# Optimization experiments

Hardware: AMD Instinct MI355X
Metric: run time of the kernel (lower is better)

## Reference

```python
import jax, jax.numpy as jnp
import numpy as np

# Model/config dims (Llama-3-8B style attention, GQA 32q/8kv)
B, S, HID = 4, 512, 4096
NH, NKV, D = 32, 8, 128
CAP = 2048          # KV cache capacity
MAXPOS = 2048       # max_position_embeddings
START = 1024        # kvcache_start_index (uniform across batch -> static masking)
EPS = 1e-6
QK_SCALE = 1.0 / float(D) ** 0.5
NEG = -1e9


def setup_inputs() -> dict:
    key = jax.random.key(0)
    ks = jax.random.split(key, 8)
    w = 0.02  # weight init scale
    return {
        'hidden_states': jax.random.normal(ks[0], (B, S, HID), jnp.float32),
        'k_cache': jax.random.normal(ks[1], (B, NKV, CAP, D), jnp.float32),
        'v_cache': jax.random.normal(ks[2], (B, NKV, CAP, D), jnp.float32),
        'rope_rotary_cos_sin': jax.random.uniform(ks[3], (B, MAXPOS, D), jnp.float32),
        'context_lengths': jnp.full((B,), S, jnp.int32),
        'kvcache_start_index': jnp.full((B,), START, jnp.int32),
        'Wq': jax.random.normal(ks[4], (HID, NH * D), jnp.float32) * w,
        'Wk': jax.random.normal(ks[5], (HID, NKV * D), jnp.float32) * w,
        'Wv': jax.random.normal(ks[6], (HID, NKV * D), jnp.float32) * w,
        'Wo': jax.random.normal(ks[7], (NH * D, HID), jnp.float32) * w,
        'q_norm_w': jnp.ones((D,), jnp.float32),
        'k_norm_w': jnp.ones((D,), jnp.float32),
    }


def _rmsnorm(x, w):
    # per-head RMSNorm over head_dim (Qwen3-style QK norm)
    return x * jax.lax.rsqrt(jnp.mean(x * x, axis=-1, keepdims=True) + EPS) * w


def _apply_rope(x, cos, sin, pos):
    # x: [B,H,S,D]; cos/sin: [MAXPOS, D/2]; pos: [B,S]
    c = cos[pos][:, None, :, :]  # [B,1,S,D/2]
    s = sin[pos][:, None, :, :]
    x1, x2 = jnp.split(x, 2, axis=-1)
    return jnp.concatenate([x1 * c - x2 * s, x2 * c + x1 * s], axis=-1)


def reference(hidden_states, k_cache, v_cache, rope_rotary_cos_sin,
              context_lengths, kvcache_start_index,
              Wq, Wk, Wv, Wo, q_norm_w, k_norm_w):
    b, s, _ = hidden_states.shape
    # fused QKV projection
    q = (hidden_states @ Wq).reshape(b, s, NH, D)
    k = (hidden_states @ Wk).reshape(b, s, NKV, D)
    v = (hidden_states @ Wv).reshape(b, s, NKV, D)
    # QK norm
    q = _rmsnorm(q, q_norm_w)
    k = _rmsnorm(k, k_norm_w)
    # [B,H,S,D]
    q = q.transpose(0, 2, 1, 3)
    k = k.transpose(0, 2, 1, 3)
    v = v.transpose(0, 2, 1, 3)
    # RoPE tables: first half cos, second half sin; batch dim 0 only
    half = D // 2
    cos = rope_rotary_cos_sin[0, :, :half]
    sin = rope_rotary_cos_sin[0, :, half:]
    pos = kvcache_start_index[:, None] + jnp.arange(s, dtype=kvcache_start_index.dtype)[None, :]
    q = _apply_rope(q, cos, sin, pos)
    k = _apply_rope(k, cos, sin, pos)
    # KV cache update: write new k/v at per-batch start index
    def upd(cache, new, st):  # cache [H,CAP,D], new [H,S,D]
        return jax.lax.dynamic_update_slice(cache, new, (0, st, 0))
    present_k = jax.vmap(upd)(k_cache, k, kvcache_start_index)
    present_v = jax.vmap(upd)(v_cache, v, kvcache_start_index)
    # GQA: expand kv heads to attention heads
    g = NH // NKV
    kf = jnp.repeat(present_k, g, axis=1)  # [B,NH,CAP,D]
    vf = jnp.repeat(present_v, g, axis=1)
    # scaled attention over cache; mask cols beyond absolute query position
    scores = jnp.einsum('bhsd,bhtd->bhst', q * QK_SCALE, kf)
    col = jnp.arange(CAP, dtype=pos.dtype)
    allowed = col[None, None, :] <= pos[:, :, None]        # [B,S,CAP]
    scores = jnp.where(allowed[:, None, :, :], scores, NEG)
    attn = jax.nn.softmax(scores, axis=-1)
    out = jnp.einsum('bhst,bhtd->bhsd', attn, vf)
    out = out.transpose(0, 2, 1, 3).reshape(b, s, NH * D)
    out = out @ Wo
    return out, present_k, present_v
```

## Files before the change

### kernel.cpp

```cpp
#include <hip/hip_runtime.h>
#include <hip/hip_bf16.h>
#include <cstdint>

#define Bsz   4
#define Ssz   512
#define HIDsz 4096
#define NHsz  32
#define NKVsz 8
#define Dsz   128
#define CAPsz 2048
#define EPSf  1e-6f
#define QK_SCALEf 0.08838834764831845f

typedef __attribute__((ext_vector_type(8))) short short8;
typedef __attribute__((ext_vector_type(4))) float f32x4;

__device__ __forceinline__ unsigned short f2bf(float x) {
    unsigned u = __float_as_uint(x);
    return (unsigned short)((u + 0x7fffu + ((u >> 16) & 1u)) >> 16);
}

__device__ __forceinline__ void gload16(const void* g, void* l) {
    __builtin_amdgcn_global_load_lds(
        (const __attribute__((address_space(1))) unsigned int*)g,
        (__attribute__((address_space(3))) unsigned int*)l, 16, 0, 0);
}

__global__ __launch_bounds__(256) void convert_bf16_kernel(
    const float* __restrict__ in, unsigned short* __restrict__ out, int n4)
{
    int i = blockIdx.x * blockDim.x + threadIdx.x;
    if (i < n4) {
        float4 v = ((const float4*)in)[i];
        ushort4 o;
        o.x = f2bf(v.x); o.y = f2bf(v.y); o.z = f2bf(v.z); o.w = f2bf(v.w);
        ((ushort4*)out)[i] = o;
    }
}

__global__ __launch_bounds__(256) void convert_k_prefix_kernel(
    const float* __restrict__ in, unsigned short* __restrict__ out,
    const int* __restrict__ start_idx)
{
    int i = blockIdx.x * blockDim.x + threadIdx.x;
    int pos = (i >> 5) & (CAPsz - 1);
    int b   = i >> 19;
    if (pos >= start_idx[b]) return;
    float4 v = ((const float4*)in)[i];
    ushort4 o;
    o.x = f2bf(v.x); o.y = f2bf(v.y); o.z = f2bf(v.z); o.w = f2bf(v.w);
    ((ushort4*)out)[i] = o;
}

__global__ __launch_bounds__(256) void transpose_bf16_kernel(
    const float* __restrict__ W, unsigned short* __restrict__ Wt, int K, int N)
{
    __shared__ float tile[64][65];
    const int k0 = blockIdx.y * 64, n0 = blockIdx.x * 64;
    const int t = threadIdx.x;
    const int tr = t >> 4, tc4 = (t & 15) * 4;
#pragma unroll
    for (int i = 0; i < 4; i++) {
        int r = tr + i * 16;
        float4 v = *(const float4*)(W + (size_t)(k0 + r) * N + n0 + tc4);
        tile[r][tc4 + 0] = v.x; tile[r][tc4 + 1] = v.y;
        tile[r][tc4 + 2] = v.z; tile[r][tc4 + 3] = v.w;
    }
    __syncthreads();
#pragma unroll
    for (int i = 0; i < 4; i++) {
        int nr = tr + i * 16;
        ushort4 o;
        o.x = f2bf(tile[tc4 + 0][nr]);
        o.y = f2bf(tile[tc4 + 1][nr]);
        o.z = f2bf(tile[tc4 + 2][nr]);
        o.w = f2bf(tile[tc4 + 3][nr]);
        *(ushort4*)(Wt + (size_t)(n0 + nr) * K + k0 + tc4) = o;
    }
}

__global__ __launch_bounds__(256) void transpose_wqkv_kernel(
    const float* __restrict__ Wq, const float* __restrict__ Wk,
    const float* __restrict__ Wv, unsigned short* __restrict__ Wt)
{
    __shared__ float tile[64][65];
    const int nt = blockIdx.x;
    const int k0 = blockIdx.y * 64;
    const float* W; int srcN, c0;
    if (nt < 64)      { W = Wq; srcN = 4096; c0 = nt * 64; }
    else if (nt < 80) { W = Wk; srcN = 1024; c0 = (nt - 64) * 64; }
    else              { W = Wv; srcN = 1024; c0 = (nt - 80) * 64; }
    const int t = threadIdx.x;
    const int tr = t >> 4, tc4 = (t & 15) * 4;
#pragma unroll
    for (int i = 0; i < 4; i++) {
        int r = tr + i * 16;
        float4 v = *(const float4*)(W + (size_t)(k0 + r) * srcN + c0 + tc4);
        tile[r][tc4 + 0] = v.x; tile[r][tc4 + 1] = v.y;
        tile[r][tc4 + 2] = v.z; tile[r][tc4 + 3] = v.w;
    }
    __syncthreads();
    const int n0 = nt * 64;
#pragma unroll
    for (int i = 0; i < 4; i++) {
        int nr = tr + i * 16;
        ushort4 o;
        o.x = f2bf(tile[tc4 + 0][nr]);
        o.y = f2bf(tile[tc4 + 1][nr]);
        o.z = f2bf(tile[tc4 + 2][nr]);
        o.w = f2bf(tile[tc4 + 3][nr]);
        *(ushort4*)(Wt + (size_t)(n0 + nr) * HIDsz + k0 + tc4) = o;
    }
}

__global__ __launch_bounds__(256) void transpose_v_kernel(
    const float* __restrict__ V, unsigned short* __restrict__ Vt,
    const int* __restrict__ start_idx)
{
    __shared__ float tile[64][65];
    const int c0 = blockIdx.x * 64, d0 = blockIdx.y * 64, bk = blockIdx.z;
    if (c0 >= start_idx[bk >> 3] + Ssz) return;
    const int t = threadIdx.x;
    const int tr = t >> 4, tc4 = (t & 15) * 4;
    const float* base = V + (size_t)bk * CAPsz * Dsz;
#pragma unroll
    for (int i = 0; i < 4; i++) {
        int r = tr + i * 16;
        float4 v = *(const float4*)(base + (size_t)(c0 + r) * Dsz + d0 + tc4);
        tile[r][tc4 + 0] = v.x; tile[r][tc4 + 1] = v.y;
        tile[r][tc4 + 2] = v.z; tile[r][tc4 + 3] = v.w;
    }
    __syncthreads();
    unsigned short* ob = Vt + (size_t)bk * Dsz * CAPsz;
#pragma unroll
    for (int i = 0; i < 4; i++) {
        int dr = tr + i * 16;
        ushort4 o;
        o.x = f2bf(tile[tc4 + 0][dr]);
        o.y = f2bf(tile[tc4 + 1][dr]);
        o.z = f2bf(tile[tc4 + 2][dr]);
        o.w = f2bf(tile[tc4 + 3][dr]);
        *(ushort4*)(ob + (size_t)(d0 + dr) * CAPsz + c0 + tc4) = o;
    }
}

__global__ __launch_bounds__(256, 3) void gemm_bf16_kernel(
    const unsigned short* __restrict__ A,
    const unsigned short* __restrict__ Bt,
    float* __restrict__ C, int M, int N, int K)
{
    __shared__ __align__(16) unsigned short As[128 * 64];
    __shared__ __align__(16) unsigned short Bs[128 * 64];
    const int t    = threadIdx.x;
    const int lane = t & 63, wv = t >> 6;
    const int m0 = blockIdx.y * 128, n0 = blockIdx.x * 128;
    const int rw = (wv & 1) * 64, cw = (wv >> 1) * 64;

    f32x4 acc[4][4];
#pragma unroll
    for (int r = 0; r < 4; r++)
#pragma unroll
        for (int c = 0; c < 4; c++) acc[r][c] = (f32x4){0.f, 0.f, 0.f, 0.f};

    const int arow = lane >> 3;
    const int acol = (lane & 7) * 8;
    const int fr = lane & 15, fq = (lane >> 4) * 8;

    for (int k0 = 0; k0 < K; k0 += 64) {
        __syncthreads();
#pragma unroll
        for (int i = 0; i < 4; i++) {
            int ro = (i * 4 + wv) * 8;
            gload16(A  + (size_t)(m0 + ro + arow) * K + k0 + acol, As + (size_t)ro * 64);
            gload16(Bt + (size_t)(n0 + ro + arow) * K + k0 + acol, Bs + (size_t)ro * 64);
        }
        __syncthreads();
#pragma unroll
        for (int kk = 0; kk < 2; kk++) {
            short8 af[4], bfr[4];
#pragma unroll
            for (int r = 0; r < 4; r++)
                af[r] = *(const short8*)&As[(rw + r * 16 + fr) * 64 + kk * 32 + fq];
#pragma unroll
            for (int c = 0; c < 4; c++)
                bfr[c] = *(const short8*)&Bs[(cw + c * 16 + fr) * 64 + kk * 32 + fq];
#pragma unroll
            for (int r = 0; r < 4; r++)
#pragma unroll
                for (int c = 0; c < 4; c++)
                    acc[r][c] = __builtin_amdgcn_mfma_f32_16x16x32_bf16(
                        af[r], bfr[c], acc[r][c], 0, 0, 0);
        }
    }

#pragma unroll
    for (int r = 0; r < 4; r++) {
#pragma unroll
        for (int c = 0; c < 4; c++) {
            int col = n0 + cw + c * 16 + (lane & 15);
#pragma unroll
            for (int reg = 0; reg < 4; reg++) {
                int row = m0 + rw + r * 16 + (lane >> 4) * 4 + reg;
                C[(size_t)row * N + col] = acc[r][c][reg];
            }
        }
    }
}

__global__ __launch_bounds__(256, 3) void gemm_qkv_kernel(
    const unsigned short* __restrict__ A,
    const unsigned short* __restrict__ Bt,
    unsigned short* __restrict__ Qout,
    float* __restrict__ Ck,
    float* __restrict__ Cv,
    unsigned short* __restrict__ Kbf,
    const float* __restrict__ rope,
    const float* __restrict__ qw,
    const float* __restrict__ knw,
    const int* __restrict__ start_idx)
{
    __shared__ __align__(16) unsigned short As[128 * 64];
    __shared__ __align__(16) unsigned short Bs[128 * 64];
    __shared__ float ssbuf[256];
    __shared__ float xbuf[256 * 17];
    const int t    = threadIdx.x;
    const int lane = t & 63, wv = t >> 6;
    const int m0 = blockIdx.y * 128, n0 = blockIdx.x * 128;
    const int rw = (wv & 1) * 64, cw = (wv >> 1) * 64;
    const int l15 = lane & 15, l4 = lane >> 4;

    f32x4 acc[4][4];
#pragma unroll
    for (int r = 0; r < 4; r++)
#pragma unroll
        for (int c = 0; c < 4; c++) acc[r][c] = (f32x4){0.f, 0.f, 0.f, 0.f};

    const int arow = lane >> 3;
    const int acol = (lane & 7) * 8;
    const int fr = l15, fq = l4 * 8;

    for (int k0 = 0; k0 < HIDsz; k0 += 64) {
        __syncthreads();
#pragma unroll
        for (int i = 0; i < 4; i++) {
            int ro = (i * 4 + wv) * 8;
            gload16(A  + (size_t)(m0 + ro + arow) * HIDsz + k0 + acol, As + (size_t)ro * 64);
            gload16(Bt + (size_t)(n0 + ro + arow) * HIDsz + k0 + acol, Bs + (size_t)ro * 64);
        }
        __syncthreads();
#pragma unroll
        for (int kk = 0; kk < 2; kk++) {
            short8 af[4], bfr[4];
#pragma unroll
            for (int r = 0; r < 4; r++)
                af[r] = *(const short8*)&As[(rw + r * 16 + fr) * 64 + kk * 32 + fq];
#pragma unroll
            for (int c = 0; c < 4; c++)
                bfr[c] = *(const short8*)&Bs[(cw + c * 16 + fr) * 64 + kk * 32 + fq];
#pragma unroll
            for (int r = 0; r < 4; r++)
#pragma unroll
                for (int c = 0; c < 4; c++)
                    acc[r][c] = __builtin_amdgcn_mfma_f32_16x16x32_bf16(
                        af[r], bfr[c], acc[r][c], 0, 0, 0);
        }
    }

    const int m0b  = m0 & (Ssz - 1);
    const int bat  = m0 >> 9;
    const int pos0 = start_idx[bat];

    if (n0 >= 5120) {
#pragma unroll
        for (int r = 0; r < 4; r++) {
#pragma unroll
            for (int c = 0; c < 4; c++) {
                int cc = (n0 - 5120) + cw + c * 16 + l15;
                int kvh = cc >> 7, d = cc & 127;
#pragma unroll
                for (int reg = 0; reg < 4; reg++) {
                    int srow = rw + r * 16 + l4 * 4 + reg;
                    int pos = pos0 + m0b + srow;
                    Cv[((size_t)(bat * NKVsz + kvh) * CAPsz + pos) * Dsz + d] = acc[r][c][reg];
                }
            }
        }
        return;
    }

    const bool isQ = (n0 < 4096);
    const float* w = isQ ? qw : knw;

#pragma unroll
    for (int r = 0; r < 4; r++)
#pragma unroll
        for (int reg = 0; reg < 4; reg++) {
            float p = acc[r][0][reg] * acc[r][0][reg]
                    + acc[r][1][reg] * acc[r][1][reg]
                    + acc[r][2][reg] * acc[r][2][reg]
                    + acc[r][3][reg] * acc[r][3][reg];
#pragma unroll
            for (int off = 1; off < 16; off <<= 1) p += __shfl_xor(p, off);
            if (l15 == 0)
                ssbuf[(rw + r * 16 + l4 * 4 + reg) * 2 + (cw >> 6)] = p;
        }
    __syncthreads();

    float wv4[4];
#pragma unroll
    for (int c = 0; c < 4; c++) wv4[c] = w[cw + c * 16 + l15];

    float rn[4][4];
#pragma unroll
    for (int r = 0; r < 4; r++)
#pragma unroll
        for (int reg = 0; reg < 4; reg++) {
            int srow = rw + r * 16 + l4 * 4 + reg;
            rn[r][reg] = rsqrtf((ssbuf[srow * 2] + ssbuf[srow * 2 + 1]) * (1.f / 128.f) + EPSf);
        }

    const int kvh = isQ ? 0 : ((n0 - 4096) >> 7);

#pragma unroll
    for (int r = 0; r < 4; r++) {
        float xn[4][4];
#pragma unroll
        for (int c = 0; c < 4; c++)
#pragma unroll
            for (int reg = 0; reg < 4; reg++) {
                xn[c][reg] = acc[r][c][reg] * rn[r][reg] * wv4[c];
                xbuf[t * 17 + c * 4 + reg] = xn[c][reg];
            }
        __syncthreads();
        float xp[4][4];
#pragma unroll
        for (int c = 0; c < 4; c++)
#pragma unroll
            for (int reg = 0; reg < 4; reg++)
                xp[c][reg] = xbuf[(t ^ 128) * 17 + c * 4 + reg];

#pragma unroll
        for (int reg = 0; reg < 4; reg++) {
            int srow = rw + r * 16 + l4 * 4 + reg;
            int pos = pos0 + m0b + srow;
            const float* rb = rope + (size_t)pos * Dsz;
#pragma unroll
            for (int c = 0; c < 4; c++) {
                int dh = cw + c * 16 + l15;
                int j = dh & 63;
                float co = rb[j], si = rb[64 + j];
                float o = (cw == 0) ? xn[c][reg] * co - xp[c][reg] * si
                                    : xn[c][reg] * co + xp[c][reg] * si;
                if (isQ) {
                    Qout[(size_t)(m0 + srow) * 4096 + n0 + dh] = f2bf(o * QK_SCALEf);
                } else {
                    size_t off = ((size_t)(bat * NKVsz + kvh) * CAPsz + pos) * Dsz + dh;
                    Ck[off]  = o;
                    Kbf[off] = f2bf(o);
                }
            }
        }
        __syncthreads();
    }
}

__global__ __launch_bounds__(256, 2) void attn_mfma_kernel(
    const unsigned short* __restrict__ Qbf,
    const unsigned short* __restrict__ Kbf,
    const unsigned short* __restrict__ Vtbf,
    unsigned short* __restrict__ O,
    const int* __restrict__ start_idx)
{
    __shared__ __align__(16) unsigned short Ks[64 * 128];
    __shared__ __align__(16) unsigned short Vs[128 * 64];
    __shared__ __align__(16) unsigned short Ps[4][32 * 72];

    const int t = threadIdx.x, lane = t & 63, wv = t >> 6;
    const int l15 = lane & 15, l4 = lane >> 4;
    const int qt = blockIdx.x, kv = blockIdx.y, b = blockIdx.z;
    const int h = kv * 4 + wv;
    const int s0 = qt * 32;
    const int start = start_idx[b];

    const int swz = (l15 & 7) << 3;

    short8 aq[2][4];
    const unsigned short* qb = Qbf + ((size_t)(b * Ssz + s0)) * HIDsz + h * Dsz;
#pragma unroll
    for (int m2 = 0; m2 < 2; m2++)
#pragma unroll
        for (int kq = 0; kq < 4; kq++)
            aq[m2][kq] = *(const short8*)(qb + (size_t)(m2 * 16 + l15) * HIDsz + kq * 32 + l4 * 8);

    f32x4 Oacc[2][8];
    float m_run[2][4], l_run[2][4];
#pragma unroll
    for (int m2 = 0; m2 < 2; m2++) {
#pragma unroll
        for (int nd = 0; nd < 8; nd++) Oacc[m2][nd] = (f32x4){0.f, 0.f, 0.f, 0.f};
#pragma unroll
        for (int r = 0; r < 4; r++) { m_run[m2][r] = -1e30f; l_run[m2][r] = 0.f; }
    }

    const unsigned short* kb = Kbf + (size_t)(b * NKVsz + kv) * CAPsz * Dsz;
    const unsigned short* vb = Vtbf + (size_t)(b * NKVsz + kv) * (size_t)Dsz * CAPsz;

    int t_hi = start + s0 + 31;
    if (t_hi > CAPsz - 1) t_hi = CAPsz - 1;

    int krow[4], vrow[4];
    unsigned short* kw[4];
    unsigned short* vw[4];
#pragma unroll
    for (int i = 0; i < 4; i++) {
        int kr = (i * 4 + wv) * 4 + l4;
        krow[i] = kr;
        kw[i] = &Ks[kr * 128 + ((l15 * 8) ^ ((kr & 7) << 3))];
        int vr = (i * 4 + wv) * 8 + (lane >> 3);
        vrow[i] = vr;
        vw[i] = &Vs[vr * 64 + (((lane & 7) * 8) ^ ((vr & 7) << 3))];
    }

    short8 kreg[4], vreg[4];
#pragma unroll
    for (int i = 0; i < 4; i++) {
        kreg[i] = *(const short8*)(kb + (size_t)krow[i] * Dsz + l15 * 8);
        vreg[i] = *(const short8*)(vb + (size_t)vrow[i] * CAPsz + (lane & 7) * 8);
    }

    for (int t0 = 0; t0 <= t_hi; t0 += 64) {
        asm volatile("s_waitcnt lgkmcnt(0)" ::: "memory");
        __builtin_amdgcn_s_barrier();
        __builtin_amdgcn_sched_barrier(0);

#pragma unroll
        for (int i = 0; i < 4; i++) *(short8*)kw[i] = kreg[i];
#pragma unroll
        for (int i = 0; i < 4; i++) *(short8*)vw[i] = vreg[i];

        if (t0 + 64 <= t_hi) {
            int tn = t0 + 64;
#pragma unroll
            for (int i = 0; i < 4; i++) {
                kreg[i] = *(const short8*)(kb + (size_t)(tn + krow[i]) * Dsz + l15 * 8);
                vreg[i] = *(const short8*)(vb + (size_t)vrow[i] * CAPsz + tn + (lane & 7) * 8);
            }
        }

        asm volatile("s_waitcnt lgkmcnt(0)" ::: "memory");
        __builtin_amdgcn_s_barrier();
        __builtin_amdgcn_sched_barrier(0);

        f32x4 Sacc[2][4];
#pragma unroll
        for (int m2 = 0; m2 < 2; m2++)
#pragma unroll
            for (int n = 0; n < 4; n++) Sacc[m2][n] = (f32x4){0.f, 0.f, 0.f, 0.f};
        __builtin_amdgcn_s_setprio(1);
#pragma unroll
        for (int kq = 0; kq < 4; kq++) {
            short8 bk[4];
#pragma unroll
            for (int n = 0; n < 4; n++)
                bk[n] = *(const short8*)&Ks[(n * 16 + l15) * 128 + ((kq * 32 + l4 * 8) ^ swz)];
#pragma unroll
            for (int m2 = 0; m2 < 2; m2++)
#pragma unroll
                for (int n = 0; n < 4; n++)
                    Sacc[m2][n] = __builtin_amdgcn_mfma_f32_16x16x32_bf16(
                        aq[m2][kq], bk[n], Sacc[m2][n], 0, 0, 0);
        }
        __builtin_amdgcn_s_setprio(0);

        bool need_mask = (t0 + 63) > (start + s0);
#pragma unroll
        for (int m2 = 0; m2 < 2; m2++) {
#pragma unroll
            for (int reg = 0; reg < 4; reg++) {
                int rloc = m2 * 16 + l4 * 4 + reg;
                int row_pos = start + s0 + rloc;
                float sv[4];
#pragma unroll
                for (int n = 0; n < 4; n++) {
                    sv[n] = Sacc[m2][n][reg];
                    if (need_mask && (t0 + n * 16 + l15 > row_pos)) sv[n] = -1e30f;
                }
                float mrow = fmaxf(fmaxf(sv[0], sv[1]), fmaxf(sv[2], sv[3]));
#pragma unroll
                for (int off = 1; off < 16; off <<= 1)
                    mrow = fmaxf(mrow, __shfl_xor(mrow, off));
                float m_new = fmaxf(m_run[m2][reg], mrow);
                float alpha = __expf(m_run[m2][reg] - m_new);
                float ps = 0.f;
#pragma unroll
                for (int n = 0; n < 4; n++) {
                    sv[n] = __expf(sv[n] - m_new);
                    ps += sv[n];
                }
#pragma unroll
                for (int off = 1; off < 16; off <<= 1)
                    ps += __shfl_xor(ps, off);
                l_run[m2][reg] = l_run[m2][reg] * alpha + ps;
                m_run[m2][reg] = m_new;
#pragma unroll
                for (int nd = 0; nd < 8; nd++) Oacc[m2][nd][reg] *= alpha;
#pragma unroll
                for (int n = 0; n < 4; n++)
                    Ps[wv][rloc * 72 + n * 16 + l15] = f2bf(sv[n]);
            }
        }

        __builtin_amdgcn_s_setprio(1);
#pragma unroll
        for (int kp = 0; kp < 2; kp++) {
            short8 ap[2];
#pragma unroll
            for (int m2 = 0; m2 < 2; m2++)
                ap[m2] = *(const short8*)&Ps[wv][(m2 * 16 + l15) * 72 + kp * 32 + l4 * 8];
#pragma unroll
            for (int nd = 0; nd < 8; nd++) {
                short8 bv = *(const short8*)&Vs[(nd * 16 + l15) * 64 + ((kp * 32 + l4 * 8) ^ swz)];
#pragma unroll
                for (int m2 = 0; m2 < 2; m2++)
                    Oacc[m2][nd] = __builtin_amdgcn_mfma_f32_16x16x32_bf16(
                        ap[m2], bv, Oacc[m2][nd], 0, 0, 0);
            }
        }
        __builtin_amdgcn_s_setprio(0);
    }

    unsigned short* ob = O + ((size_t)(b * Ssz + s0)) * HIDsz + h * Dsz;
#pragma unroll
    for (int m2 = 0; m2 < 2; m2++)
#pragma unroll
        for (int reg = 0; reg < 4; reg++) {
            int rloc = m2 * 16 + l4 * 4 + reg;
            float inv = 1.f / l_run[m2][reg];
#pragma unroll
            for (int nd = 0; nd < 8; nd++)
                ob[(size_t)rloc * HIDsz + nd * 16 + l15] = f2bf(Oacc[m2][nd][reg] * inv);
        }
}

extern "C" void kernel_launch(void* const* d_in, const int* in_sizes, int n_in,
                              void* d_out, int out_size, void* d_ws, size_t ws_size,
                              hipStream_t stream) {
    (void)in_sizes; (void)n_in; (void)out_size; (void)ws_size;
    const float* hidden    = (const float*)d_in[0];
    const float* k_cache   = (const float*)d_in[1];
    const float* v_cache   = (const float*)d_in[2];
    const float* rope      = (const float*)d_in[3];
    const int*   start_idx = (const int*)d_in[5];
    const float* Wq        = (const float*)d_in[6];
    const float* Wk        = (const float*)d_in[7];
    const float* Wv        = (const float*)d_in[8];
    const float* Wo        = (const float*)d_in[9];
    const float* q_norm_w  = (const float*)d_in[10];
    const float* k_norm_w  = (const float*)d_in[11];

    float* out   = (float*)d_out;
    float* out_k = out + (size_t)Bsz * Ssz * HIDsz;
    float* out_v = out_k + (size_t)Bsz * NKVsz * CAPsz * Dsz;

    char* ws = (char*)d_ws;
    unsigned short* Kbf       = (unsigned short*)ws;
    unsigned short* Vtbf      = (unsigned short*)(ws + (((size_t) 16) << 20));
    unsigned short* hidden_bf = (unsigned short*)(ws + (((size_t) 32) << 20));
    unsigned short* attn_bf   = (unsigned short*)(ws + (((size_t) 48) << 20));
    unsigned short* qbf       = (unsigned short*)(ws + (((size_t) 64) << 20));
    unsigned short* Wqkv_t    = (unsigned short*)(ws + (((size_t) 80) << 20));
    unsigned short* Wo_t      = Wqkv_t;

    const size_t cache_bytes = (size_t)Bsz * NKVsz * CAPsz * Dsz * sizeof(float);
    (void)hipMemcpyAsync(out_k, k_cache, cache_bytes, hipMemcpyDeviceToDevice, stream);
    (void)hipMemcpyAsync(out_v, v_cache, cache_bytes, hipMemcpyDeviceToDevice, stream);

    convert_bf16_kernel<<<8192, 256, 0, stream>>>(hidden, hidden_bf, 2048 * 4096 / 4);
    transpose_wqkv_kernel<<<dim3(96, 64), 256, 0, stream>>>(Wq, Wk, Wv, Wqkv_t);

    gemm_qkv_kernel<<<dim3(48, 16), 256, 0, stream>>>(
        hidden_bf, Wqkv_t, qbf, out_k, out_v, Kbf, rope,
        q_norm_w, k_norm_w, start_idx);

    convert_k_prefix_kernel<<<8192, 256, 0, stream>>>(out_k, Kbf, start_idx);
    transpose_v_kernel<<<dim3(32, 2, 32), 256, 0, stream>>>(out_v, Vtbf, start_idx);

    attn_mfma_kernel<<<dim3(16, NKVsz, Bsz), 256, 0, stream>>>(qbf, Kbf, Vtbf, attn_bf, start_idx);

    transpose_bf16_kernel<<<dim3(64, 64), 256, 0, stream>>>(Wo, Wo_t, NHsz * Dsz, HIDsz);
    gemm_bf16_kernel<<<dim3(32, 16), 256, 0, stream>>>(attn_bf, Wo_t, out, 2048, 4096, 4096);
}
```

Measured before the change: 662.3 us.

## Split attention KV range across two blocks and merge with combine kernel

Each query tile's KV range is split into two halves processed by separate blocks, doubling the attention grid. Each block writes partial normalized outputs plus running max and sum, and a new combine kernel merges them with log-sum-exp weights. The launch bound is raised to target three blocks per CU. This aims to fix underfilled CUs and causal load imbalance, at the cost of an extra pass over the bf16 output and extra rounding of the partial results.

```diff
diff --git a/kernel.cpp b/kernel.cpp
--- a/kernel.cpp
+++ b/kernel.cpp
@@ -18,6 +18,9 @@
 __device__ __forceinline__ unsigned short f2bf(float x) {
     unsigned u = __float_as_uint(x);
     return (unsigned short)((u + 0x7fffu + ((u >> 16) & 1u)) >> 16);
+}
+__device__ __forceinline__ float bf2f(unsigned short u) {
+    return __uint_as_float(((unsigned)u) << 16);
 }
 
 __device__ __forceinline__ void gload16(const void* g, void* l) {
@@ -364,11 +367,14 @@
     }
 }
 
-__global__ __launch_bounds__(256, 2) void attn_mfma_kernel(
+__global__ __launch_bounds__(256, 3) void attn_mfma_kernel(
     const unsigned short* __restrict__ Qbf,
     const unsigned short* __restrict__ Kbf,
     const unsigned short* __restrict__ Vtbf,
-    unsigned short* __restrict__ O,
+    unsigned short* __restrict__ O0,
+    unsigned short* __restrict__ O1,
+    float2* __restrict__ ML0,
+    float2* __restrict__ ML1,
     const int* __restrict__ start_idx)
 {
     __shared__ __align__(16) unsigned short Ks[64 * 128];
@@ -377,20 +383,16 @@
 
     const int t = threadIdx.x, lane = t & 63, wv = t >> 6;
     const int l15 = lane & 15, l4 = lane >> 4;
-    const int qt = blockIdx.x, kv = blockIdx.y, b = blockIdx.z;
+    const int qt = blockIdx.x >> 1, half = blockIdx.x & 1;
+    const int kv = blockIdx.y, b = blockIdx.z;
     const int h = kv * 4 + wv;
     const int s0 = qt * 32;
     const int start = start_idx[b];
 
+    unsigned short* Oh = half ? O1 : O0;
+    float2*         MLh = half ? ML1 : ML0;
+
     const int swz = (l15 & 7) << 3;
-
-    short8 aq[2][4];
-    const unsigned short* qb = Qbf + ((size_t)(b * Ssz + s0)) * HIDsz + h * Dsz;
-#pragma unroll
-    for (int m2 = 0; m2 < 2; m2++)
-#pragma unroll
-        for (int kq = 0; kq < 4; kq++)
-            aq[m2][kq] = *(const short8*)(qb + (size_t)(m2 * 16 + l15) * HIDsz + kq * 32 + l4 * 8);
 
     f32x4 Oacc[2][8];
     float m_run[2][4], l_run[2][4];
@@ -402,144 +404,186 @@
         for (int r = 0; r < 4; r++) { m_run[m2][r] = -1e30f; l_run[m2][r] = 0.f; }
     }
 
-    const unsigned short* kb = Kbf + (size_t)(b * NKVsz + kv) * CAPsz * Dsz;
-    const unsigned short* vb = Vtbf + (size_t)(b * NKVsz + kv) * (size_t)Dsz * CAPsz;
-
     int t_hi = start + s0 + 31;
     if (t_hi > CAPsz - 1) t_hi = CAPsz - 1;
-
-    int krow[4], vrow[4];
-    unsigned short* kw[4];
-    unsigned short* vw[4];
-#pragma unroll
-    for (int i = 0; i < 4; i++) {
-        int kr = (i * 4 + wv) * 4 + l4;
-        krow[i] = kr;
-        kw[i] = &Ks[kr * 128 + ((l15 * 8) ^ ((kr & 7) << 3))];
-        int vr = (i * 4 + wv) * 8 + (lane >> 3);
-        vrow[i] = vr;
-        vw[i] = &Vs[vr * 64 + (((lane & 7) * 8) ^ ((vr & 7) << 3))];
-    }
-
-    short8 kreg[4], vreg[4];
-#pragma unroll
-    for (int i = 0; i < 4; i++) {
-        kreg[i] = *(const short8*)(kb + (size_t)krow[i] * Dsz + l15 * 8);
-        vreg[i] = *(const short8*)(vb + (size_t)vrow[i] * CAPsz + (lane & 7) * 8);
-    }
-
-    for (int t0 = 0; t0 <= t_hi; t0 += 64) {
-        asm volatile("s_waitcnt lgkmcnt(0)" ::: "memory");
-        __builtin_amdgcn_s_barrier();
-        __builtin_amdgcn_sched_barrier(0);
-
-#pragma unroll
-        for (int i = 0; i < 4; i++) *(short8*)kw[i] = kreg[i];
-#pragma unroll
-        for (int i = 0; i < 4; i++) *(short8*)vw[i] = vreg[i];
-
-        if (t0 + 64 <= t_hi) {
-            int tn = t0 + 64;
-#pragma unroll
-            for (int i = 0; i < 4; i++) {
-                kreg[i] = *(const short8*)(kb + (size_t)(tn + krow[i]) * Dsz + l15 * 8);
-                vreg[i] = *(const short8*)(vb + (size_t)vrow[i] * CAPsz + tn + (lane & 7) * 8);
-            }
-        }
-
-        asm volatile("s_waitcnt lgkmcnt(0)" ::: "memory");
-        __builtin_amdgcn_s_barrier();
-        __builtin_amdgcn_sched_barrier(0);
-
-        f32x4 Sacc[2][4];
+    const int ntiles = (t_hi >> 6) + 1;
+    const int nh0 = (ntiles + 1) >> 1;
+    const int tile_lo = half ? nh0 : 0;
+    const int tile_hi = half ? ntiles : nh0;
+    const int tstart = tile_lo << 6;
+    const int tend   = tile_hi << 6;
+
+    if (tile_lo < tile_hi) {
+        short8 aq[2][4];
+        const unsigned short* qb = Qbf + ((size_t)(b * Ssz + s0)) * HIDsz + h * Dsz;
 #pragma unroll
         for (int m2 = 0; m2 < 2; m2++)
 #pragma unroll
-            for (int n = 0; n < 4; n++) Sacc[m2][n] = (f32x4){0.f, 0.f, 0.f, 0.f};
-        __builtin_amdgcn_s_setprio(1);
-#pragma unroll
-        for (int kq = 0; kq < 4; kq++) {
-            short8 bk[4];
-#pragma unroll
-            for (int n = 0; n < 4; n++)
-                bk[n] = *(const short8*)&Ks[(n * 16 + l15) * 128 + ((kq * 32 + l4 * 8) ^ swz)];
+            for (int kq = 0; kq < 4; kq++)
+                aq[m2][kq] = *(const short8*)(qb + (size_t)(m2 * 16 + l15) * HIDsz + kq * 32 + l4 * 8);
+
+        const unsigned short* kb = Kbf + (size_t)(b * NKVsz + kv) * CAPsz * Dsz;
+        const unsigned short* vb = Vtbf + (size_t)(b * NKVsz + kv) * (size_t)Dsz * CAPsz;
+
+        int krow[4], vrow[4];
+        unsigned short* kw[4];
+        unsigned short* vw[4];
+#pragma unroll
+        for (int i = 0; i < 4; i++) {
+            int kr = (i * 4 + wv) * 4 + l4;
+            krow[i] = kr;
+            kw[i] = &Ks[kr * 128 + ((l15 * 8) ^ ((kr & 7) << 3))];
+            int vr = (i * 4 + wv) * 8 + (lane >> 3);
+            vrow[i] = vr;
+            vw[i] = &Vs[vr * 64 + (((lane & 7) * 8) ^ ((vr & 7) << 3))];
+        }
+
+        short8 kreg[4], vreg[4];
+#pragma unroll
+        for (int i = 0; i < 4; i++) {
+            kreg[i] = *(const short8*)(kb + (size_t)(tstart + krow[i]) * Dsz + l15 * 8);
+            vreg[i] = *(const short8*)(vb + (size_t)vrow[i] * CAPsz + tstart + (lane & 7) * 8);
+        }
+
+        for (int t0 = tstart; t0 < tend; t0 += 64) {
+            asm volatile("s_waitcnt lgkmcnt(0)" ::: "memory");
+            __builtin_amdgcn_s_barrier();
+            __builtin_amdgcn_sched_barrier(0);
+
+#pragma unroll
+            for (int i = 0; i < 4; i++) *(short8*)kw[i] = kreg[i];
+#pragma unroll
+            for (int i = 0; i < 4; i++) *(short8*)vw[i] = vreg[i];
+
+            if (t0 + 64 < tend) {
+                int tn = t0 + 64;
+#pragma unroll
+                for (int i = 0; i < 4; i++) {
+                    kreg[i] = *(const short8*)(kb + (size_t)(tn + krow[i]) * Dsz + l15 * 8);
+                    vreg[i] = *(const short8*)(vb + (size_t)vrow[i] * CAPsz + tn + (lane & 7) * 8);
+                }
+            }
+
+            asm volatile("s_waitcnt lgkmcnt(0)" ::: "memory");
+            __builtin_amdgcn_s_barrier();
+            __builtin_amdgcn_sched_barrier(0);
+
+            f32x4 Sacc[2][4];
 #pragma unroll
             for (int m2 = 0; m2 < 2; m2++)
 #pragma unroll
+                for (int n = 0; n < 4; n++) Sacc[m2][n] = (f32x4){0.f, 0.f, 0.f, 0.f};
+            __builtin_amdgcn_s_setprio(1);
+#pragma unroll
+            for (int kq = 0; kq < 4; kq++) {
+                short8 bk[4];
+#pragma unroll
                 for (int n = 0; n < 4; n++)
-                    Sacc[m2][n] = __builtin_amdgcn_mfma_f32_16x16x32_bf16(
-                        aq[m2][kq], bk[n], Sacc[m2][n], 0, 0, 0);
-        }
-        __builtin_amdgcn_s_setprio(0);
-
-        bool need_mask = (t0 + 63) > (start + s0);
-#pragma unroll
-        for (int m2 = 0; m2 < 2; m2++) {
-#pragma unroll
-            for (int reg = 0; reg < 4; reg++) {
-                int rloc = m2 * 16 + l4 * 4 + reg;
-                int row_pos = start + s0 + rloc;
-                float sv[4];
-#pragma unroll
-                for (int n = 0; n < 4; n++) {
-                    sv[n] = Sacc[m2][n][reg];
-                    if (need_mask && (t0 + n * 16 + l15 > row_pos)) sv[n] = -1e30f;
+                    bk[n] = *(const short8*)&Ks[(n * 16 + l15) * 128 + ((kq * 32 + l4 * 8) ^ swz)];
+#pragma unroll
+                for (int m2 = 0; m2 < 2; m2++)
+#pragma unroll
+                    for (int n = 0; n < 4; n++)
+                        Sacc[m2][n] = __builtin_amdgcn_mfma_f32_16x16x32_bf16(
+                            aq[m2][kq], bk[n], Sacc[m2][n], 0, 0, 0);
+            }
+            __builtin_amdgcn_s_setprio(0);
+
+            bool need_mask = (t0 + 63) > (start + s0);
+#pragma unroll
+            for (int m2 = 0; m2 < 2; m2++) {
+#pragma unroll
+                for (int reg = 0; reg < 4; reg++) {
+                    int rloc = m2 * 16 + l4 * 4 + reg;
+                    int row_pos = start + s0 + rloc;
+                    float sv[4];
+#pragma unroll
+                    for (int n = 0; n < 4; n++) {
+                        sv[n] = Sacc[m2][n][reg];
+                        if (need_mask && (t0 + n * 16 + l15 > row_pos)) sv[n] = -1e30f;
+                    }
+                    float mrow = fmaxf(fmaxf(sv[0], sv[1]), fmaxf(sv[2], sv[3]));
+#pragma unroll
+                    for (int off = 1; off < 16; off <<= 1)
+                        mrow = fmaxf(mrow, __shfl_xor(mrow, off));
+                    float m_new = fmaxf(m_run[m2][reg], mrow);
+                    float alpha = __expf(m_run[m2][reg] - m_new);
+                    float ps = 0.f;
+#pragma unroll
+                    for (int n = 0; n < 4; n++) {
+                        sv[n] = __expf(sv[n] - m_new);
+                        ps += sv[n];
+                    }
+#pragma unroll
+                    for (int off = 1; off < 16; off <<= 1)
+                        ps += __shfl_xor(ps, off);
+                    l_run[m2][reg] = l_run[m2][reg] * alpha + ps;
+                    m_run[m2][reg] = m_new;
+#pragma unroll
+                    for (int nd = 0; nd < 8; nd++) Oacc[m2][nd][reg] *= alpha;
+#pragma unroll
+                    for (int n = 0; n < 4; n++)
+                        Ps[wv][rloc * 72 + n * 16 + l15] = f2bf(sv[n]);
                 }
-                float mrow = fmaxf(fmaxf(sv[0], sv[1]), fmaxf(sv[2], sv[3]));
-#pragma unroll
-                for (int off = 1; off < 16; off <<= 1)
-                    mrow = fmaxf(mrow, __shfl_xor(mrow, off));
-                float m_new = fmaxf(m_run[m2][reg], mrow);
-                float alpha = __expf(m_run[m2][reg] - m_new);
-                float ps = 0.f;
-#pragma unroll
-                for (int n = 0; n < 4; n++) {
-                    sv[n] = __expf(sv[n] - m_new);
-                    ps += sv[n];
+            }
+
+            __builtin_amdgcn_s_setprio(1);
+#pragma unroll
+            for (int kp = 0; kp < 2; kp++) {
+                short8 ap[2];
+#pragma unroll
+                for (int m2 = 0; m2 < 2; m2++)
+                    ap[m2] = *(const short8*)&Ps[wv][(m2 * 16 + l15) * 72 + kp * 32 + l4 * 8];
+#pragma unroll
+                for (int nd = 0; nd < 8; nd++) {
+                    short8 bv = *(const short8*)&Vs[(nd * 16 + l15) * 64 + ((kp * 32 + l4 * 8) ^ swz)];
+#pragma unroll
+                    for (int m2 = 0; m2 < 2; m2++)
+                        Oacc[m2][nd] = __builtin_amdgcn_mfma_f32_16x16x32_bf16(
+                            ap[m2], bv, Oacc[m2][nd], 0, 0, 0);
                 }
-#pragma unroll
-                for (int off = 1; off < 16; off <<= 1)
-                    ps += __shfl_xor(ps, off);
-                l_run[m2][reg] = l_run[m2][reg] * alpha + ps;
-                m_run[m2][reg] = m_new;
-#pragma unroll
-                for (int nd = 0; nd < 8; nd++) Oacc[m2][nd][reg] *= alpha;
-#pragma unroll
-                for (int n = 0; n < 4; n++)
-                    Ps[wv][rloc * 72 + n * 16 + l15] = f2bf(sv[n]);
-            }
-        }
-
-        __builtin_amdgcn_s_setprio(1);
-#pragma unroll
-        for (int kp = 0; kp < 2; kp++) {
-            short8 ap[2];
-#pragma unroll
-            for (int m2 = 0; m2 < 2; m2++)
-                ap[m2] = *(const short8*)&Ps[wv][(m2 * 16 + l15) * 72 + kp * 32 + l4 * 8];
-#pragma unroll
-            for (int nd = 0; nd < 8; nd++) {
-                short8 bv = *(const short8*)&Vs[(nd * 16 + l15) * 64 + ((kp * 32 + l4 * 8) ^ swz)];
-#pragma unroll
-                for (int m2 = 0; m2 < 2; m2++)
-                    Oacc[m2][nd] = __builtin_amdgcn_mfma_f32_16x16x32_bf16(
-                        ap[m2], bv, Oacc[m2][nd], 0, 0, 0);
-            }
-        }
-        __builtin_amdgcn_s_setprio(0);
-    }
-
-    unsigned short* ob = O + ((size_t)(b * Ssz + s0)) * HIDsz + h * Dsz;
+            }
+            __builtin_amdgcn_s_setprio(0);
+        }
+    }
+
+    unsigned short* ob = Oh + ((size_t)(b * Ssz + s0)) * HIDsz + h * Dsz;
 #pragma unroll
     for (int m2 = 0; m2 < 2; m2++)
 #pragma unroll
         for (int reg = 0; reg < 4; reg++) {
             int rloc = m2 * 16 + l4 * 4 + reg;
-            float inv = 1.f / l_run[m2][reg];
+            float lr = l_run[m2][reg];
+            float inv = lr > 0.f ? 1.f / lr : 0.f;
 #pragma unroll
             for (int nd = 0; nd < 8; nd++)
                 ob[(size_t)rloc * HIDsz + nd * 16 + l15] = f2bf(Oacc[m2][nd][reg] * inv);
-        }
+            if (l15 == 0)
+                MLh[((size_t)(b * Ssz + s0 + rloc)) * NHsz + h] =
+                    make_float2(m_run[m2][reg], lr);
+        }
+}
+
+__global__ __launch_bounds__(256) void attn_combine_kernel(
+    unsigned short* __restrict__ O0, const unsigned short* __restrict__ O1,
+    const float2* __restrict__ ML0, const float2* __restrict__ ML1)
+{
+    int i = blockIdx.x * blockDim.x + threadIdx.x;
+    int th = i >> 5;
+    float2 a = ML0[th], c = ML1[th];
+    float M = fmaxf(a.x, c.x);
+    float w0 = a.y * __expf(a.x - M);
+    float w1 = c.y * __expf(c.x - M);
+    float inv = 1.f / (w0 + w1);
+    w0 *= inv; w1 *= inv;
+    ushort4 u0 = ((const ushort4*)O0)[i];
+    ushort4 u1 = ((const ushort4*)O1)[i];
+    ushort4 o;
+    o.x = f2bf(w0 * bf2f(u0.x) + w1 * bf2f(u1.x));
+    o.y = f2bf(w0 * bf2f(u0.y) + w1 * bf2f(u1.y));
+    o.z = f2bf(w0 * bf2f(u0.z) + w1 * bf2f(u1.z));
+    o.w = f2bf(w0 * bf2f(u0.w) + w1 * bf2f(u1.w));
+    ((ushort4*)O0)[i] = o;
 }
 
 extern "C" void kernel_launch(void* const* d_in, const int* in_sizes, int n_in,
@@ -570,6 +614,9 @@
     unsigned short* qbf       = (unsigned short*)(ws + (((size_t) 64) << 20));
     unsigned short* Wqkv_t    = (unsigned short*)(ws + (((size_t) 80) << 20));
     unsigned short* Wo_t      = Wqkv_t;
+    unsigned short* O1        = hidden_bf;
+    float2*         ML0       = (float2*)(ws + (((size_t)112) << 20));
+    float2*         ML1       = (float2*)(ws + (((size_t)113) << 20));
 
     const size_t cache_bytes = (size_t)Bsz * NKVsz * CAPsz * Dsz * sizeof(float);
     (void)hipMemcpyAsync(out_k, k_cache, cache_bytes, hipMemcpyDeviceToDevice, stream);
@@ -585,7 +632,9 @@
     convert_k_prefix_kernel<<<8192, 256, 0, stream>>>(out_k, Kbf, start_idx);
     transpose_v_kernel<<<dim3(32, 2, 32), 256, 0, stream>>>(out_v, Vtbf, start_idx);
 
-    attn_mfma_kernel<<<dim3(16, NKVsz, Bsz), 256, 0, stream>>>(qbf, Kbf, Vtbf, attn_bf, start_idx);
+    attn_mfma_kernel<<<dim3(32, NKVsz, Bsz), 256, 0, stream>>>(
+        qbf, Kbf, Vtbf, attn_bf, O1, ML0, ML1, start_idx);
+    attn_combine_kernel<<<8192, 256, 0, stream>>>(attn_bf, O1, ML0, ML1);
 
     transpose_bf16_kernel<<<dim3(64, 64), 256, 0, stream>>>(Wo, Wo_t, NHsz * Dsz, HIDsz);
     gemm_bf16_kernel<<<dim3(32, 16), 256, 0, stream>>>(attn_bf, Wo_t, out, 2048, 4096, 4096);
```

New measurement: 875.0 us. 1.32x slower.
